# Performance work log

Measured on AMD Instinct MI355X. Metric: run time of the kernel, lower is better.

## Reference

```python
import jax, jax.numpy as jnp
import numpy as np

N = 100000
E = 3200000
D_IN = 128
HEADS = 4
OUT_CH = 64


def setup_inputs() -> dict:
    key = jax.random.key(0)
    kx, ke, kw, kb = jax.random.split(key, 4)
    x = jax.random.normal(kx, (N, D_IN), dtype=jnp.float32)
    edge_index = jax.random.randint(ke, (2, E), 0, N, dtype=jnp.int64)
    # nn.Linear(in_channels, out_channels*heads): weight [out, in] in torch; store as [in, out] for x @ W
    W = jax.random.normal(kw, (D_IN, OUT_CH * HEADS), dtype=jnp.float32) * (1.0 / np.sqrt(D_IN))
    b = jax.random.normal(kb, (OUT_CH * HEADS,), dtype=jnp.float32) * 0.01
    return {"x": x, "edge_index": edge_index, "W": W, "b": b}


def reference(x, edge_index, W, b):
    src, dst = edge_index[0], edge_index[1]
    n = x.shape[0]
    # scatter-add of gathered src features into dst rows (segment sum)
    agg = jax.ops.segment_sum(x[src], dst, num_segments=n)  # [N, D_IN]
    count = jax.ops.segment_sum(jnp.ones((src.shape[0], 1), x.dtype), dst, num_segments=n)  # [N, 1]
    agg = agg / (count + 1e-8)
    # linear on (x + agg); view to [N, heads*out_channels] is a no-op reshape
    return (x + agg) @ W + b
```

## Files before the change

### kernel.cpp

```cpp
#include <hip/hip_runtime.h>

#define N_NODES 100000
#define D_IN 128
#define D_OUT 256
#define NBLK 512
#define NBKT 2048
#define BSH  6
#define BNODES 64
#define NBUCKETS ((N_NODES + BNODES - 1) / BNODES)
#define CAP  3072

typedef __attribute__((ext_vector_type(8))) short short8_t;
typedef __attribute__((ext_vector_type(4))) float f32x4;

__device__ inline unsigned short f2bf_rne(float f) {
    unsigned u = __float_as_uint(f);
    u += 0x7fffu + ((u >> 16) & 1u);
    return (unsigned short)(u >> 16);
}

__global__ __launch_bounds__(256) void convert_kernel(
    const float* __restrict__ x, ushort* __restrict__ xb, int n4)
{
    int i = blockIdx.x * 256 + threadIdx.x;
    if (i < n4) {
        float4 v = ((const float4*)x)[i];
        ushort4 r;
        r.x = f2bf_rne(v.x); r.y = f2bf_rne(v.y);
        r.z = f2bf_rne(v.z); r.w = f2bf_rne(v.w);
        ((ushort4*)xb)[i] = r;
    }
}

__global__ __launch_bounds__(256) void wfrag_kernel(
    const float* __restrict__ W, short8_t* __restrict__ wfrag)
{
    int tid  = blockIdx.x * 256 + threadIdx.x;
    int lane = tid & 63;
    int fi   = tid >> 6;
    int ks   = fi >> 4, nt = fi & 15;
    int k0   = ks * 32 + (lane >> 4) * 8;
    int col  = nt * 16 + (lane & 15);
    short8_t v;
    #pragma unroll
    for (int e = 0; e < 8; e++)
        v[e] = (short)f2bf_rne(W[(size_t)(k0 + e) * D_OUT + col]);
    wfrag[tid] = v;
}

__global__ __launch_bounds__(256) void binA_hist(
    const int* __restrict__ dst, int* __restrict__ blockHist, int E, int chunk)
{
    __shared__ int h[NBKT];
    int b = blockIdx.x, t = threadIdx.x;
    for (int i = t; i < NBKT; i += 256) h[i] = 0;
    __syncthreads();
    int e0 = b * chunk, e1 = min(e0 + chunk, E);
    for (int e = e0 + t; e < e1; e += 256)
        atomicAdd(&h[dst[e] >> BSH], 1);
    __syncthreads();
    for (int i = t; i < NBKT; i += 256)
        blockHist[b * NBKT + i] = h[i];
}

__global__ __launch_bounds__(256) void binA_scan(
    int* __restrict__ blockHist, int* __restrict__ bucketTotal)
{
    __shared__ int wsum[4];
    int bucket = blockIdx.x;
    int t = threadIdx.x, lane = t & 63, w = t >> 6;
    int v0 = blockHist[(t * 2    ) * NBKT + bucket];
    int v1 = blockHist[(t * 2 + 1) * NBKT + bucket];
    int v = v0 + v1;
    int s = v;
    #pragma unroll
    for (int d = 1; d < 64; d <<= 1) {
        int u = __shfl_up(s, d);
        if (lane >= d) s += u;
    }
    if (lane == 63) wsum[w] = s;
    __syncthreads();
    int wo = 0;
    for (int j = 0; j < w; j++) wo += wsum[j];
    int excl = wo + s - v;
    blockHist[(t * 2    ) * NBKT + bucket] = excl;
    blockHist[(t * 2 + 1) * NBKT + bucket] = excl + v0;
    if (t == 255) {
        int tot = 0;
        for (int j = 0; j < 4; j++) tot += wsum[j];
        bucketTotal[bucket] = tot;
    }
}

__global__ __launch_bounds__(256) void binA_scanbase(
    const int* __restrict__ bucketTotal, int* __restrict__ bucketBase)
{
    __shared__ int wsum[4];
    int t = threadIdx.x, lane = t & 63, w = t >> 6;
    int i0 = t * 8;
    int a[8], v = 0;
    #pragma unroll
    for (int j = 0; j < 8; j++) { a[j] = bucketTotal[i0 + j]; v += a[j]; }
    int s = v;
    #pragma unroll
    for (int d = 1; d < 64; d <<= 1) {
        int u = __shfl_up(s, d);
        if (lane >= d) s += u;
    }
    if (lane == 63) wsum[w] = s;
    __syncthreads();
    int wo = 0;
    for (int j = 0; j < w; j++) wo += wsum[j];
    int excl = wo + s - v;
    #pragma unroll
    for (int j = 0; j < 8; j++) { bucketBase[i0 + j] = excl; excl += a[j]; }
}

__global__ __launch_bounds__(256) void binA_scatter(
    const int* __restrict__ src, const int* __restrict__ dst,
    const int* __restrict__ blockHist, const int* __restrict__ bucketBase,
    unsigned* __restrict__ pairs, int E, int chunk)
{
    __shared__ int offs[NBKT];
    int b = blockIdx.x, t = threadIdx.x;
    for (int i = t; i < NBKT; i += 256)
        offs[i] = bucketBase[i] + blockHist[b * NBKT + i];
    __syncthreads();
    int e0 = b * chunk, e1 = min(e0 + chunk, E);
    for (int e = e0 + t; e < e1; e += 256) {
        int d = dst[e];
        int bin = d >> BSH;
        int pos = atomicAdd(&offs[bin], 1);
        pairs[pos] = ((unsigned)(d & (BNODES - 1)) << 17) | (unsigned)src[e];
    }
}

__global__ __launch_bounds__(256) void binB_sort(
    unsigned* __restrict__ pairs, const int* __restrict__ bucketBase,
    int* __restrict__ offs_g, int* __restrict__ deg_g)
{
    __shared__ unsigned stage[CAP];
    __shared__ int hist[256];
    __shared__ int rank[256];
    __shared__ int wsum[4];

    int b = blockIdx.x, t = threadIdx.x, lane = t & 63, w = t >> 6;
    int e0 = bucketBase[b], e1 = bucketBase[b + 1];
    int cnt = e1 - e0;
    if (cnt > CAP) cnt = CAP;

    hist[t] = 0;
    __syncthreads();

    for (int i = t; i < cnt; i += 256) {
        unsigned p = pairs[e0 + i];
        stage[i] = p;
        atomicAdd(&hist[p >> 17], 1);
    }
    __syncthreads();

    int v = hist[t];
    int s = v;
    #pragma unroll
    for (int d = 1; d < 64; d <<= 1) {
        int u = __shfl_up(s, d);
        if (lane >= d) s += u;
    }
    if (lane == 63) wsum[w] = s;
    __syncthreads();
    int wo = 0;
    for (int j = 0; j < w; j++) wo += wsum[j];
    int excl = wo + s - v;

    int node = (b << BSH) + t;
    if (t < BNODES && node < N_NODES) {
        offs_g[node] = e0 + excl;
        deg_g[node]  = v;
    }
    rank[t] = excl;
    __syncthreads();

    for (int i = t; i < cnt; i += 256) {
        unsigned p = stage[i];
        int pos = atomicAdd(&rank[p >> 17], 1);
        pairs[e0 + pos] = p & 0x1FFFFu;
    }
}

template <bool USE_BF16>
__global__ __launch_bounds__(256) void fused_kernel(
    const float* __restrict__ x,
    const ushort* __restrict__ xb,
    const int* __restrict__ offs,
    const int* __restrict__ deg,
    const int* __restrict__ sorted_src,
    const short8_t* __restrict__ wfrag,
    const float* __restrict__ b,
    float* __restrict__ out)
{
    __shared__ __align__(16) ushort shb[16 * D_IN];

    int n0   = blockIdx.x * 16;
    int t    = threadIdx.x;
    int lane = t & 63;
    int w    = t >> 6;

    for (int nn = 0; nn < 4; nn++) {
        int nl = w * 4 + nn;
        int n  = n0 + nl;
        int start = offs[n];
        int d     = deg[n];
        float accx = 0.0f, accy = 0.0f;
        for (int base = 0; base < d; base += 64) {
            int m = d - base; if (m > 64) m = 64;
            int id = (lane < m) ? sorted_src[start + base + lane] : 0;
            int j = 0;
            for (; j + 4 <= m; j += 4) {
                int s0 = __builtin_amdgcn_readlane(id, j);
                int s1 = __builtin_amdgcn_readlane(id, j + 1);
                int s2 = __builtin_amdgcn_readlane(id, j + 2);
                int s3 = __builtin_amdgcn_readlane(id, j + 3);
                if (USE_BF16) {
                    ushort2 u0 = ((const ushort2*)(xb + (size_t)s0 * D_IN))[lane];
                    ushort2 u1 = ((const ushort2*)(xb + (size_t)s1 * D_IN))[lane];
                    ushort2 u2 = ((const ushort2*)(xb + (size_t)s2 * D_IN))[lane];
                    ushort2 u3 = ((const ushort2*)(xb + (size_t)s3 * D_IN))[lane];
                    accx += __uint_as_float((unsigned)u0.x << 16)
                          + __uint_as_float((unsigned)u1.x << 16)
                          + __uint_as_float((unsigned)u2.x << 16)
                          + __uint_as_float((unsigned)u3.x << 16);
                    accy += __uint_as_float((unsigned)u0.y << 16)
                          + __uint_as_float((unsigned)u1.y << 16)
                          + __uint_as_float((unsigned)u2.y << 16)
                          + __uint_as_float((unsigned)u3.y << 16);
                } else {
                    float2 v0 = ((const float2*)(x + (size_t)s0 * D_IN))[lane];
                    float2 v1 = ((const float2*)(x + (size_t)s1 * D_IN))[lane];
                    float2 v2 = ((const float2*)(x + (size_t)s2 * D_IN))[lane];
                    float2 v3 = ((const float2*)(x + (size_t)s3 * D_IN))[lane];
                    accx += v0.x + v1.x + v2.x + v3.x;
                    accy += v0.y + v1.y + v2.y + v3.y;
                }
            }
            for (; j < m; j++) {
                int s0 = __builtin_amdgcn_readlane(id, j);
                if (USE_BF16) {
                    ushort2 u0 = ((const ushort2*)(xb + (size_t)s0 * D_IN))[lane];
                    accx += __uint_as_float((unsigned)u0.x << 16);
                    accy += __uint_as_float((unsigned)u0.y << 16);
                } else {
                    float2 v0 = ((const float2*)(x + (size_t)s0 * D_IN))[lane];
                    accx += v0.x; accy += v0.y;
                }
            }
        }
        float invc = 1.0f / ((float)d + 1e-8f);
        float2 xv = ((const float2*)(x + (size_t)n * D_IN))[lane];
        float hx = xv.x + accx * invc;
        float hy = xv.y + accy * invc;
        unsigned hp = ((unsigned)f2bf_rne(hy) << 16) | (unsigned)f2bf_rne(hx);
        unsigned byteoff = ((unsigned)(nl * 256 + lane * 4)) ^ (((unsigned)nl & 7u) << 4);
        *(unsigned*)((char*)shb + byteoff) = hp;
    }
    __syncthreads();

    const int r  = lane & 15;
    const int hi = lane >> 4;

    short8_t afrag[4];
    #pragma unroll
    for (int ks = 0; ks < 4; ks++) {
        unsigned aoff = ((unsigned)(r * 256 + ks * 64 + hi * 16)) ^ (((unsigned)r & 7u) << 4);
        afrag[ks] = *(const short8_t*)((const char*)shb + aoff);
    }

    f32x4 zero = {0.0f, 0.0f, 0.0f, 0.0f};
    f32x4 acc0 = zero, acc1 = zero, acc2 = zero, acc3 = zero;
    const int nt0 = w * 4;
    #pragma unroll
    for (int ks = 0; ks < 4; ks++) {
        short8_t b0 = wfrag[(ks * 16 + nt0    ) * 64 + lane];
        short8_t b1 = wfrag[(ks * 16 + nt0 + 1) * 64 + lane];
        short8_t b2 = wfrag[(ks * 16 + nt0 + 2) * 64 + lane];
        short8_t b3 = wfrag[(ks * 16 + nt0 + 3) * 64 + lane];
        acc0 = __builtin_amdgcn_mfma_f32_16x16x32_bf16(afrag[ks], b0, acc0, 0, 0, 0);
        acc1 = __builtin_amdgcn_mfma_f32_16x16x32_bf16(afrag[ks], b1, acc1, 0, 0, 0);
        acc2 = __builtin_amdgcn_mfma_f32_16x16x32_bf16(afrag[ks], b2, acc2, 0, 0, 0);
        acc3 = __builtin_amdgcn_mfma_f32_16x16x32_bf16(afrag[ks], b3, acc3, 0, 0, 0);
    }

    #pragma unroll
    for (int nt = 0; nt < 4; nt++) {
        f32x4 a = (nt == 0) ? acc0 : (nt == 1) ? acc1 : (nt == 2) ? acc2 : acc3;
        int col = (nt0 + nt) * 16 + r;
        float bias = b[col];
        #pragma unroll
        for (int reg = 0; reg < 4; reg++) {
            int node = n0 + hi * 4 + reg;
            out[(size_t)node * D_OUT + col] = a[reg] + bias;
        }
    }
}

extern "C" void kernel_launch(void* const* d_in, const int* in_sizes, int n_in,
                              void* d_out, int out_size, void* d_ws, size_t ws_size,
                              hipStream_t stream)
{
    const float* x  = (const float*)d_in[0];
    const int*   ei = (const int*)d_in[1];
    const float* W  = (const float*)d_in[2];
    const float* b  = (const float*)d_in[3];
    float*       out = (float*)d_out;

    const int E = in_sizes[1] / 2;
    const int* src = ei;
    const int* dst = ei + E;
    const int chunk = (E + NBLK - 1) / NBLK;

    const size_t xb_bytes   = (size_t)N_NODES * D_IN * 2;
    const size_t pairs_b    = (size_t)E * 4;
    const size_t bh_b       = (size_t)NBLK * NBKT * 4;
    const size_t small_b    = (size_t)NBKT * 4;
    const size_t nodes_b    = (size_t)N_NODES * 4;
    const size_t wf_b       = (size_t)4096 * 16;
    const size_t need_bf16  = xb_bytes + pairs_b + bh_b + 2 * small_b
                            + 2 * nodes_b + wf_b;
    const bool use_bf16 = (ws_size >= need_bf16);

    char* p = (char*)d_ws;
    ushort* xb = nullptr;
    if (use_bf16) { xb = (ushort*)p; p += xb_bytes; }
    unsigned* pairs  = (unsigned*)p;  p += pairs_b;
    int* blockHist   = (int*)p;       p += bh_b;
    int* bucketTotal = (int*)p;       p += small_b;
    int* bucketBase  = (int*)p;       p += small_b;
    int* offs        = (int*)p;       p += nodes_b;
    int* deg         = (int*)p;       p += nodes_b;
    short8_t* wfrag  = (short8_t*)p;

    if (use_bf16) {
        int n4 = N_NODES * D_IN / 4;
        convert_kernel<<<dim3((n4 + 255) / 256), dim3(256), 0, stream>>>(x, xb, n4);
    }
    wfrag_kernel<<<dim3(16), dim3(256), 0, stream>>>(W, wfrag);

    binA_hist    <<<dim3(NBLK), dim3(256), 0, stream>>>(dst, blockHist, E, chunk);
    binA_scan    <<<dim3(NBKT), dim3(256), 0, stream>>>(blockHist, bucketTotal);
    binA_scanbase<<<dim3(1),    dim3(256), 0, stream>>>(bucketTotal, bucketBase);
    binA_scatter <<<dim3(NBLK), dim3(256), 0, stream>>>(
        src, dst, blockHist, bucketBase, pairs, E, chunk);
    binB_sort    <<<dim3(NBUCKETS), dim3(256), 0, stream>>>(
        pairs, bucketBase, offs, deg);

    if (use_bf16)
        fused_kernel<true><<<dim3(N_NODES / 16), dim3(256), 0, stream>>>(
            x, xb, offs, deg, (const int*)pairs, wfrag, b, out);
    else
        fused_kernel<false><<<dim3(N_NODES / 16), dim3(256), 0, stream>>>(
            x, xb, offs, deg, (const int*)pairs, wfrag, b, out);
}
```

Baseline: 408.7 us.

## Fuse per-bucket sort into aggregation kernel, one block per 64-node bucket

Removes the separate binB_sort kernel and does the per-bucket counting sort in LDS inside the fused aggregation+GEMM kernel. Each block now handles one 64-node bucket (16 nodes per wave) and no longer writes or rereads offs/deg arrays or the sorted pairs from global memory. In exchange, LDS use per block rises (CAP ints plus a 64x128 bf16 tile), which may lower occupancy, and the block count drops from 6250 to about 1563. Each wave now runs 16 MFMA column tiles with the B fragments loaded per tile.

```diff
diff --git a/kernel.cpp b/kernel.cpp
--- a/kernel.cpp
+++ b/kernel.cpp
@@ -135,85 +135,68 @@
     }
 }
 
-__global__ __launch_bounds__(256) void binB_sort(
-    unsigned* __restrict__ pairs, const int* __restrict__ bucketBase,
-    int* __restrict__ offs_g, int* __restrict__ deg_g)
-{
-    __shared__ unsigned stage[CAP];
-    __shared__ int hist[256];
-    __shared__ int rank[256];
-    __shared__ int wsum[4];
-
-    int b = blockIdx.x, t = threadIdx.x, lane = t & 63, w = t >> 6;
-    int e0 = bucketBase[b], e1 = bucketBase[b + 1];
-    int cnt = e1 - e0;
-    if (cnt > CAP) cnt = CAP;
-
-    hist[t] = 0;
-    __syncthreads();
-
-    for (int i = t; i < cnt; i += 256) {
-        unsigned p = pairs[e0 + i];
-        stage[i] = p;
-        atomicAdd(&hist[p >> 17], 1);
-    }
-    __syncthreads();
-
-    int v = hist[t];
-    int s = v;
-    #pragma unroll
-    for (int d = 1; d < 64; d <<= 1) {
-        int u = __shfl_up(s, d);
-        if (lane >= d) s += u;
-    }
-    if (lane == 63) wsum[w] = s;
-    __syncthreads();
-    int wo = 0;
-    for (int j = 0; j < w; j++) wo += wsum[j];
-    int excl = wo + s - v;
-
-    int node = (b << BSH) + t;
-    if (t < BNODES && node < N_NODES) {
-        offs_g[node] = e0 + excl;
-        deg_g[node]  = v;
-    }
-    rank[t] = excl;
-    __syncthreads();
-
-    for (int i = t; i < cnt; i += 256) {
-        unsigned p = stage[i];
-        int pos = atomicAdd(&rank[p >> 17], 1);
-        pairs[e0 + pos] = p & 0x1FFFFu;
-    }
-}
-
 template <bool USE_BF16>
 __global__ __launch_bounds__(256) void fused_kernel(
     const float* __restrict__ x,
     const ushort* __restrict__ xb,
-    const int* __restrict__ offs,
-    const int* __restrict__ deg,
-    const int* __restrict__ sorted_src,
+    const unsigned* __restrict__ pairs,
+    const int* __restrict__ bucketBase,
     const short8_t* __restrict__ wfrag,
     const float* __restrict__ b,
     float* __restrict__ out)
 {
-    __shared__ __align__(16) ushort shb[16 * D_IN];
-
-    int n0   = blockIdx.x * 16;
-    int t    = threadIdx.x;
-    int lane = t & 63;
-    int w    = t >> 6;
-
-    for (int nn = 0; nn < 4; nn++) {
-        int nl = w * 4 + nn;
+    __shared__ int srcSorted[CAP];
+    __shared__ __align__(16) ushort shb[BNODES * D_IN];
+    __shared__ int hist_l[BNODES];
+    __shared__ int offs_l[BNODES];
+    __shared__ int rank_l[BNODES];
+
+    const int t    = threadIdx.x;
+    const int lane = t & 63;
+    const int w    = t >> 6;
+    const int bkt  = blockIdx.x;
+    const int n0   = bkt << BSH;
+
+    const int e0 = bucketBase[bkt], e1 = bucketBase[bkt + 1];
+    int cnt = e1 - e0;
+    if (cnt > CAP) cnt = CAP;
+
+    if (t < BNODES) hist_l[t] = 0;
+    __syncthreads();
+
+    for (int i = t; i < cnt; i += 256)
+        atomicAdd(&hist_l[pairs[e0 + i] >> 17], 1);
+    __syncthreads();
+
+    if (t < 64) {
+        int v = hist_l[t];
+        int s = v;
+        #pragma unroll
+        for (int d = 1; d < 64; d <<= 1) {
+            int u = __shfl_up(s, d);
+            if (t >= d) s += u;
+        }
+        offs_l[t] = s - v;
+        rank_l[t] = s - v;
+    }
+    __syncthreads();
+
+    for (int i = t; i < cnt; i += 256) {
+        unsigned p = pairs[e0 + i];
+        int pos = atomicAdd(&rank_l[p >> 17], 1);
+        srcSorted[pos] = (int)(p & 0x1FFFFu);
+    }
+    __syncthreads();
+
+    for (int nn = 0; nn < 16; nn++) {
+        int nl = (w << 4) + nn;
         int n  = n0 + nl;
-        int start = offs[n];
-        int d     = deg[n];
+        int start = offs_l[nl];
+        int d     = hist_l[nl];
         float accx = 0.0f, accy = 0.0f;
         for (int base = 0; base < d; base += 64) {
             int m = d - base; if (m > 64) m = 64;
-            int id = (lane < m) ? sorted_src[start + base + lane] : 0;
+            int id = (lane < m) ? srcSorted[start + base + lane] : 0;
             int j = 0;
             for (; j + 4 <= m; j += 4) {
                 int s0 = __builtin_amdgcn_readlane(id, j);
@@ -254,10 +237,13 @@
                 }
             }
         }
-        float invc = 1.0f / ((float)d + 1e-8f);
-        float2 xv = ((const float2*)(x + (size_t)n * D_IN))[lane];
-        float hx = xv.x + accx * invc;
-        float hy = xv.y + accy * invc;
+        float hx = 0.0f, hy = 0.0f;
+        if (n < N_NODES) {
+            float invc = 1.0f / ((float)d + 1e-8f);
+            float2 xv = ((const float2*)(x + (size_t)n * D_IN))[lane];
+            hx = xv.x + accx * invc;
+            hy = xv.y + accy * invc;
+        }
         unsigned hp = ((unsigned)f2bf_rne(hy) << 16) | (unsigned)f2bf_rne(hx);
         unsigned byteoff = ((unsigned)(nl * 256 + lane * 4)) ^ (((unsigned)nl & 7u) << 4);
         *(unsigned*)((char*)shb + byteoff) = hp;
@@ -266,38 +252,30 @@
 
     const int r  = lane & 15;
     const int hi = lane >> 4;
+    const int rr = (w << 4) + r;
 
     short8_t afrag[4];
     #pragma unroll
     for (int ks = 0; ks < 4; ks++) {
-        unsigned aoff = ((unsigned)(r * 256 + ks * 64 + hi * 16)) ^ (((unsigned)r & 7u) << 4);
+        unsigned aoff = ((unsigned)(rr * 256 + ks * 64 + hi * 16)) ^ (((unsigned)rr & 7u) << 4);
         afrag[ks] = *(const short8_t*)((const char*)shb + aoff);
     }
 
-    f32x4 zero = {0.0f, 0.0f, 0.0f, 0.0f};
-    f32x4 acc0 = zero, acc1 = zero, acc2 = zero, acc3 = zero;
-    const int nt0 = w * 4;
-    #pragma unroll
-    for (int ks = 0; ks < 4; ks++) {
-        short8_t b0 = wfrag[(ks * 16 + nt0    ) * 64 + lane];
-        short8_t b1 = wfrag[(ks * 16 + nt0 + 1) * 64 + lane];
-        short8_t b2 = wfrag[(ks * 16 + nt0 + 2) * 64 + lane];
-        short8_t b3 = wfrag[(ks * 16 + nt0 + 3) * 64 + lane];
-        acc0 = __builtin_amdgcn_mfma_f32_16x16x32_bf16(afrag[ks], b0, acc0, 0, 0, 0);
-        acc1 = __builtin_amdgcn_mfma_f32_16x16x32_bf16(afrag[ks], b1, acc1, 0, 0, 0);
-        acc2 = __builtin_amdgcn_mfma_f32_16x16x32_bf16(afrag[ks], b2, acc2, 0, 0, 0);
-        acc3 = __builtin_amdgcn_mfma_f32_16x16x32_bf16(afrag[ks], b3, acc3, 0, 0, 0);
-    }
-
-    #pragma unroll
-    for (int nt = 0; nt < 4; nt++) {
-        f32x4 a = (nt == 0) ? acc0 : (nt == 1) ? acc1 : (nt == 2) ? acc2 : acc3;
-        int col = (nt0 + nt) * 16 + r;
+    #pragma unroll 4
+    for (int nt = 0; nt < 16; nt++) {
+        f32x4 acc = {0.0f, 0.0f, 0.0f, 0.0f};
+        #pragma unroll
+        for (int ks = 0; ks < 4; ks++) {
+            short8_t bf = wfrag[(ks * 16 + nt) * 64 + lane];
+            acc = __builtin_amdgcn_mfma_f32_16x16x32_bf16(afrag[ks], bf, acc, 0, 0, 0);
+        }
+        int col = nt * 16 + r;
         float bias = b[col];
         #pragma unroll
         for (int reg = 0; reg < 4; reg++) {
-            int node = n0 + hi * 4 + reg;
-            out[(size_t)node * D_OUT + col] = a[reg] + bias;
+            int node = n0 + (w << 4) + hi * 4 + reg;
+            if (node < N_NODES)
+                out[(size_t)node * D_OUT + col] = acc[reg] + bias;
         }
     }
 }
@@ -321,10 +299,8 @@
     const size_t pairs_b    = (size_t)E * 4;
     const size_t bh_b       = (size_t)NBLK * NBKT * 4;
     const size_t small_b    = (size_t)NBKT * 4;
-    const size_t nodes_b    = (size_t)N_NODES * 4;
     const size_t wf_b       = (size_t)4096 * 16;
-    const size_t need_bf16  = xb_bytes + pairs_b + bh_b + 2 * small_b
-                            + 2 * nodes_b + wf_b;
+    const size_t need_bf16  = xb_bytes + pairs_b + bh_b + 2 * small_b + wf_b;
     const bool use_bf16 = (ws_size >= need_bf16);
 
     char* p = (char*)d_ws;
@@ -334,8 +310,6 @@
     int* blockHist   = (int*)p;       p += bh_b;
     int* bucketTotal = (int*)p;       p += small_b;
     int* bucketBase  = (int*)p;       p += small_b;
-    int* offs        = (int*)p;       p += nodes_b;
-    int* deg         = (int*)p;       p += nodes_b;
     short8_t* wfrag  = (short8_t*)p;
 
     if (use_bf16) {
@@ -349,13 +323,11 @@
     binA_scanbase<<<dim3(1),    dim3(256), 0, stream>>>(bucketTotal, bucketBase);
     binA_scatter <<<dim3(NBLK), dim3(256), 0, stream>>>(
         src, dst, blockHist, bucketBase, pairs, E, chunk);
-    binB_sort    <<<dim3(NBUCKETS), dim3(256), 0, stream>>>(
-        pairs, bucketBase, offs, deg);
 
     if (use_bf16)
-        fused_kernel<true><<<dim3(N_NODES / 16), dim3(256), 0, stream>>>(
-            x, xb, offs, deg, (const int*)pairs, wfrag, b, out);
+        fused_kernel<true><<<dim3(NBUCKETS), dim3(256), 0, stream>>>(
+            x, xb, pairs, bucketBase, wfrag, b, out);
     else
-        fused_kernel<false><<<dim3(N_NODES / 16), dim3(256), 0, stream>>>(
-            x, xb, offs, deg, (const int*)pairs, wfrag, b, out);
-}
+        fused_kernel<false><<<dim3(NBUCKETS), dim3(256), 0, stream>>>(
+            x, xb, pairs, bucketBase, wfrag, b, out);
+}
```

Result: slower. 450.0 us (+10.1%).

## Replace two-level bucket sort with global-atomic counting sort for CSR build

Applied to the files above, without the earlier changes.

Replaces the two-pass bucket binning (per-block histograms, bucket scan, scatter, then in-LDS sort per bucket) with a direct CSR build. The new path counts degrees with global atomics, runs a three-stage prefix scan over nodes, and scatters src indices using per-node atomic cursors. This drops the large per-block histogram buffer and the LDS sort pass, but 3.2M global atomics on random addresses are added twice. The scatter writes are random and neighbour order within each node is nondeterministic, which can slightly change float summation order.

```diff
diff --git a/kernel.cpp b/kernel.cpp
--- a/kernel.cpp
+++ b/kernel.cpp
@@ -3,12 +3,8 @@
 #define N_NODES 100000
 #define D_IN 128
 #define D_OUT 256
-#define NBLK 512
-#define NBKT 2048
-#define BSH  6
-#define BNODES 64
-#define NBUCKETS ((N_NODES + BNODES - 1) / BNODES)
-#define CAP  3072
+#define NBLKN ((N_NODES + 255) / 256)
+#define EBLK 2048
 
 typedef __attribute__((ext_vector_type(8))) short short8_t;
 typedef __attribute__((ext_vector_type(4))) float f32x4;
@@ -48,30 +44,54 @@
     wfrag[tid] = v;
 }
 
-__global__ __launch_bounds__(256) void binA_hist(
-    const int* __restrict__ dst, int* __restrict__ blockHist, int E, int chunk)
-{
-    __shared__ int h[NBKT];
-    int b = blockIdx.x, t = threadIdx.x;
-    for (int i = t; i < NBKT; i += 256) h[i] = 0;
+__global__ __launch_bounds__(256) void zero_deg(int* __restrict__ deg)
+{
+    int i = blockIdx.x * 256 + threadIdx.x;
+    if (i < N_NODES) deg[i] = 0;
+}
+
+__global__ __launch_bounds__(256) void count_deg(
+    const int* __restrict__ dst, int* __restrict__ deg, int E)
+{
+    int stride = gridDim.x * 256;
+    for (int i = blockIdx.x * 256 + threadIdx.x; i < E; i += stride)
+        atomicAdd(&deg[dst[i]], 1);
+}
+
+__global__ __launch_bounds__(256) void scanA(
+    const int* __restrict__ deg, int* __restrict__ offs, int* __restrict__ bsum)
+{
+    __shared__ int wsum[4];
+    int b = blockIdx.x, t = threadIdx.x, lane = t & 63, w = t >> 6;
+    int n = b * 256 + t;
+    int v = (n < N_NODES) ? deg[n] : 0;
+    int s = v;
+    #pragma unroll
+    for (int d = 1; d < 64; d <<= 1) {
+        int u = __shfl_up(s, d);
+        if (lane >= d) s += u;
+    }
+    if (lane == 63) wsum[w] = s;
     __syncthreads();
-    int e0 = b * chunk, e1 = min(e0 + chunk, E);
-    for (int e = e0 + t; e < e1; e += 256)
-        atomicAdd(&h[dst[e] >> BSH], 1);
-    __syncthreads();
-    for (int i = t; i < NBKT; i += 256)
-        blockHist[b * NBKT + i] = h[i];
-}
-
-__global__ __launch_bounds__(256) void binA_scan(
-    int* __restrict__ blockHist, int* __restrict__ bucketTotal)
+    int wo = 0;
+    for (int j = 0; j < w; j++) wo += wsum[j];
+    if (n < N_NODES) offs[n] = wo + s - v;
+    if (t == 255) {
+        int tot = 0;
+        for (int j = 0; j < 4; j++) tot += wsum[j];
+        bsum[b] = tot;
+    }
+}
+
+__global__ __launch_bounds__(256) void scanB(
+    const int* __restrict__ bsum, int* __restrict__ bbase)
 {
     __shared__ int wsum[4];
-    int bucket = blockIdx.x;
     int t = threadIdx.x, lane = t & 63, w = t >> 6;
-    int v0 = blockHist[(t * 2    ) * NBKT + bucket];
-    int v1 = blockHist[(t * 2 + 1) * NBKT + bucket];
-    int v = v0 + v1;
+    int i0 = t * 2;
+    int a0 = (i0     < NBLKN) ? bsum[i0]     : 0;
+    int a1 = (i0 + 1 < NBLKN) ? bsum[i0 + 1] : 0;
+    int v = a0 + a1;
     int s = v;
     #pragma unroll
     for (int d = 1; d < 64; d <<= 1) {
@@ -83,107 +103,31 @@
     int wo = 0;
     for (int j = 0; j < w; j++) wo += wsum[j];
     int excl = wo + s - v;
-    blockHist[(t * 2    ) * NBKT + bucket] = excl;
-    blockHist[(t * 2 + 1) * NBKT + bucket] = excl + v0;
-    if (t == 255) {
-        int tot = 0;
-        for (int j = 0; j < 4; j++) tot += wsum[j];
-        bucketTotal[bucket] = tot;
-    }
-}
-
-__global__ __launch_bounds__(256) void binA_scanbase(
-    const int* __restrict__ bucketTotal, int* __restrict__ bucketBase)
-{
-    __shared__ int wsum[4];
-    int t = threadIdx.x, lane = t & 63, w = t >> 6;
-    int i0 = t * 8;
-    int a[8], v = 0;
-    #pragma unroll
-    for (int j = 0; j < 8; j++) { a[j] = bucketTotal[i0 + j]; v += a[j]; }
-    int s = v;
-    #pragma unroll
-    for (int d = 1; d < 64; d <<= 1) {
-        int u = __shfl_up(s, d);
-        if (lane >= d) s += u;
-    }
-    if (lane == 63) wsum[w] = s;
-    __syncthreads();
-    int wo = 0;
-    for (int j = 0; j < w; j++) wo += wsum[j];
-    int excl = wo + s - v;
-    #pragma unroll
-    for (int j = 0; j < 8; j++) { bucketBase[i0 + j] = excl; excl += a[j]; }
-}
-
-__global__ __launch_bounds__(256) void binA_scatter(
+    if (i0     < NBLKN) bbase[i0]     = excl;
+    if (i0 + 1 < NBLKN) bbase[i0 + 1] = excl + a0;
+}
+
+__global__ __launch_bounds__(256) void scanC(
+    int* __restrict__ offs, const int* __restrict__ bbase, int* __restrict__ cur)
+{
+    int b = blockIdx.x, t = threadIdx.x;
+    int n = b * 256 + t;
+    if (n < N_NODES) {
+        int o = offs[n] + bbase[b];
+        offs[n] = o;
+        cur[n]  = o;
+    }
+}
+
+__global__ __launch_bounds__(256) void scatter_csr(
     const int* __restrict__ src, const int* __restrict__ dst,
-    const int* __restrict__ blockHist, const int* __restrict__ bucketBase,
-    unsigned* __restrict__ pairs, int E, int chunk)
-{
-    __shared__ int offs[NBKT];
-    int b = blockIdx.x, t = threadIdx.x;
-    for (int i = t; i < NBKT; i += 256)
-        offs[i] = bucketBase[i] + blockHist[b * NBKT + i];
-    __syncthreads();
-    int e0 = b * chunk, e1 = min(e0 + chunk, E);
-    for (int e = e0 + t; e < e1; e += 256) {
-        int d = dst[e];
-        int bin = d >> BSH;
-        int pos = atomicAdd(&offs[bin], 1);
-        pairs[pos] = ((unsigned)(d & (BNODES - 1)) << 17) | (unsigned)src[e];
-    }
-}
-
-__global__ __launch_bounds__(256) void binB_sort(
-    unsigned* __restrict__ pairs, const int* __restrict__ bucketBase,
-    int* __restrict__ offs_g, int* __restrict__ deg_g)
-{
-    __shared__ unsigned stage[CAP];
-    __shared__ int hist[256];
-    __shared__ int rank[256];
-    __shared__ int wsum[4];
-
-    int b = blockIdx.x, t = threadIdx.x, lane = t & 63, w = t >> 6;
-    int e0 = bucketBase[b], e1 = bucketBase[b + 1];
-    int cnt = e1 - e0;
-    if (cnt > CAP) cnt = CAP;
-
-    hist[t] = 0;
-    __syncthreads();
-
-    for (int i = t; i < cnt; i += 256) {
-        unsigned p = pairs[e0 + i];
-        stage[i] = p;
-        atomicAdd(&hist[p >> 17], 1);
-    }
-    __syncthreads();
-
-    int v = hist[t];
-    int s = v;
-    #pragma unroll
-    for (int d = 1; d < 64; d <<= 1) {
-        int u = __shfl_up(s, d);
-        if (lane >= d) s += u;
-    }
-    if (lane == 63) wsum[w] = s;
-    __syncthreads();
-    int wo = 0;
-    for (int j = 0; j < w; j++) wo += wsum[j];
-    int excl = wo + s - v;
-
-    int node = (b << BSH) + t;
-    if (t < BNODES && node < N_NODES) {
-        offs_g[node] = e0 + excl;
-        deg_g[node]  = v;
-    }
-    rank[t] = excl;
-    __syncthreads();
-
-    for (int i = t; i < cnt; i += 256) {
-        unsigned p = stage[i];
-        int pos = atomicAdd(&rank[p >> 17], 1);
-        pairs[e0 + pos] = p & 0x1FFFFu;
+    int* __restrict__ cur, int* __restrict__ csr, int E)
+{
+    int stride = gridDim.x * 256;
+    for (int i = blockIdx.x * 256 + threadIdx.x; i < E; i += stride) {
+        int d = dst[i];
+        int pos = atomicAdd(&cur[d], 1);
+        csr[pos] = src[i];
     }
 }
 
@@ -315,28 +259,25 @@
     const int E = in_sizes[1] / 2;
     const int* src = ei;
     const int* dst = ei + E;
-    const int chunk = (E + NBLK - 1) / NBLK;
-
-    const size_t xb_bytes   = (size_t)N_NODES * D_IN * 2;
-    const size_t pairs_b    = (size_t)E * 4;
-    const size_t bh_b       = (size_t)NBLK * NBKT * 4;
-    const size_t small_b    = (size_t)NBKT * 4;
-    const size_t nodes_b    = (size_t)N_NODES * 4;
-    const size_t wf_b       = (size_t)4096 * 16;
-    const size_t need_bf16  = xb_bytes + pairs_b + bh_b + 2 * small_b
-                            + 2 * nodes_b + wf_b;
+
+    const size_t xb_bytes  = (size_t)N_NODES * D_IN * 2;
+    const size_t csr_b     = (size_t)E * 4;
+    const size_t nodes_b   = (size_t)N_NODES * 4;
+    const size_t bsum_b    = (size_t)512 * 4;
+    const size_t wf_b      = (size_t)4096 * 16;
+    const size_t need_bf16 = xb_bytes + csr_b + 3 * nodes_b + 2 * bsum_b + wf_b;
     const bool use_bf16 = (ws_size >= need_bf16);
 
     char* p = (char*)d_ws;
     ushort* xb = nullptr;
     if (use_bf16) { xb = (ushort*)p; p += xb_bytes; }
-    unsigned* pairs  = (unsigned*)p;  p += pairs_b;
-    int* blockHist   = (int*)p;       p += bh_b;
-    int* bucketTotal = (int*)p;       p += small_b;
-    int* bucketBase  = (int*)p;       p += small_b;
-    int* offs        = (int*)p;       p += nodes_b;
-    int* deg         = (int*)p;       p += nodes_b;
-    short8_t* wfrag  = (short8_t*)p;
+    int* csr   = (int*)p;  p += csr_b;
+    int* deg   = (int*)p;  p += nodes_b;
+    int* offs  = (int*)p;  p += nodes_b;
+    int* cur   = (int*)p;  p += nodes_b;
+    int* bsum  = (int*)p;  p += bsum_b;
+    int* bbase = (int*)p;  p += bsum_b;
+    short8_t* wfrag = (short8_t*)p;
 
     if (use_bf16) {
         int n4 = N_NODES * D_IN / 4;
@@ -344,18 +285,17 @@
     }
     wfrag_kernel<<<dim3(16), dim3(256), 0, stream>>>(W, wfrag);
 
-    binA_hist    <<<dim3(NBLK), dim3(256), 0, stream>>>(dst, blockHist, E, chunk);
-    binA_scan    <<<dim3(NBKT), dim3(256), 0, stream>>>(blockHist, bucketTotal);
-    binA_scanbase<<<dim3(1),    dim3(256), 0, stream>>>(bucketTotal, bucketBase);
-    binA_scatter <<<dim3(NBLK), dim3(256), 0, stream>>>(
-        src, dst, blockHist, bucketBase, pairs, E, chunk);
-    binB_sort    <<<dim3(NBUCKETS), dim3(256), 0, stream>>>(
-        pairs, bucketBase, offs, deg);
+    zero_deg   <<<dim3(NBLKN), dim3(256), 0, stream>>>(deg);
+    count_deg  <<<dim3(EBLK),  dim3(256), 0, stream>>>(dst, deg, E);
+    scanA      <<<dim3(NBLKN), dim3(256), 0, stream>>>(deg, offs, bsum);
+    scanB      <<<dim3(1),     dim3(256), 0, stream>>>(bsum, bbase);
+    scanC      <<<dim3(NBLKN), dim3(256), 0, stream>>>(offs, bbase, cur);
+    scatter_csr<<<dim3(EBLK),  dim3(256), 0, stream>>>(src, dst, cur, csr, E);
 
     if (use_bf16)
         fused_kernel<true><<<dim3(N_NODES / 16), dim3(256), 0, stream>>>(
-            x, xb, offs, deg, (const int*)pairs, wfrag, b, out);
+            x, xb, offs, deg, csr, wfrag, b, out);
     else
         fused_kernel<false><<<dim3(N_NODES / 16), dim3(256), 0, stream>>>(
-            x, xb, offs, deg, (const int*)pairs, wfrag, b, out);
-}
+            x, xb, offs, deg, csr, wfrag, b, out);
+}
```

Result: slower. 670.4 us (+64.0%).

## Use coarser 512-node buckets with fewer binning blocks for the edge sort

Applied to the files above, without the earlier changes.

The two-level counting sort of edges by destination now uses 256 buckets of 512 nodes each instead of 2048 buckets of 64 nodes, and 256 histogram blocks instead of 512. The histogram, scan and scatter kernels are simplified to one bucket per thread, and the per-bucket sort now handles 512 local nodes with a large LDS staging buffer. This cuts the block-histogram traffic and the scan work. In exchange the sort runs as only about 196 large blocks that use a lot of shared memory, and any bucket holding more than CAP edges gets truncated.

```diff
diff --git a/kernel.cpp b/kernel.cpp
--- a/kernel.cpp
+++ b/kernel.cpp
@@ -3,12 +3,12 @@
 #define N_NODES 100000
 #define D_IN 128
 #define D_OUT 256
-#define NBLK 512
-#define NBKT 2048
-#define BSH  6
-#define BNODES 64
+#define NBLK 256
+#define NBKT 256
+#define BSH  9
+#define BNODES 512
 #define NBUCKETS ((N_NODES + BNODES - 1) / BNODES)
-#define CAP  3072
+#define CAP  19456
 
 typedef __attribute__((ext_vector_type(8))) short short8_t;
 typedef __attribute__((ext_vector_type(4))) float f32x4;
@@ -53,14 +53,13 @@
 {
     __shared__ int h[NBKT];
     int b = blockIdx.x, t = threadIdx.x;
-    for (int i = t; i < NBKT; i += 256) h[i] = 0;
+    h[t] = 0;
     __syncthreads();
     int e0 = b * chunk, e1 = min(e0 + chunk, E);
     for (int e = e0 + t; e < e1; e += 256)
         atomicAdd(&h[dst[e] >> BSH], 1);
     __syncthreads();
-    for (int i = t; i < NBKT; i += 256)
-        blockHist[b * NBKT + i] = h[i];
+    blockHist[b * NBKT + t] = h[t];
 }
 
 __global__ __launch_bounds__(256) void binA_scan(
@@ -69,9 +68,7 @@
     __shared__ int wsum[4];
     int bucket = blockIdx.x;
     int t = threadIdx.x, lane = t & 63, w = t >> 6;
-    int v0 = blockHist[(t * 2    ) * NBKT + bucket];
-    int v1 = blockHist[(t * 2 + 1) * NBKT + bucket];
-    int v = v0 + v1;
+    int v = blockHist[t * NBKT + bucket];
     int s = v;
     #pragma unroll
     for (int d = 1; d < 64; d <<= 1) {
@@ -82,9 +79,7 @@
     __syncthreads();
     int wo = 0;
     for (int j = 0; j < w; j++) wo += wsum[j];
-    int excl = wo + s - v;
-    blockHist[(t * 2    ) * NBKT + bucket] = excl;
-    blockHist[(t * 2 + 1) * NBKT + bucket] = excl + v0;
+    blockHist[t * NBKT + bucket] = wo + s - v;
     if (t == 255) {
         int tot = 0;
         for (int j = 0; j < 4; j++) tot += wsum[j];
@@ -97,10 +92,7 @@
 {
     __shared__ int wsum[4];
     int t = threadIdx.x, lane = t & 63, w = t >> 6;
-    int i0 = t * 8;
-    int a[8], v = 0;
-    #pragma unroll
-    for (int j = 0; j < 8; j++) { a[j] = bucketTotal[i0 + j]; v += a[j]; }
+    int v = bucketTotal[t];
     int s = v;
     #pragma unroll
     for (int d = 1; d < 64; d <<= 1) {
@@ -111,9 +103,7 @@
     __syncthreads();
     int wo = 0;
     for (int j = 0; j < w; j++) wo += wsum[j];
-    int excl = wo + s - v;
-    #pragma unroll
-    for (int j = 0; j < 8; j++) { bucketBase[i0 + j] = excl; excl += a[j]; }
+    bucketBase[t] = wo + s - v;
 }
 
 __global__ __launch_bounds__(256) void binA_scatter(
@@ -123,8 +113,7 @@
 {
     __shared__ int offs[NBKT];
     int b = blockIdx.x, t = threadIdx.x;
-    for (int i = t; i < NBKT; i += 256)
-        offs[i] = bucketBase[i] + blockHist[b * NBKT + i];
+    offs[t] = bucketBase[t] + blockHist[b * NBKT + t];
     __syncthreads();
     int e0 = b * chunk, e1 = min(e0 + chunk, E);
     for (int e = e0 + t; e < e1; e += 256) {
@@ -140,8 +129,8 @@
     int* __restrict__ offs_g, int* __restrict__ deg_g)
 {
     __shared__ unsigned stage[CAP];
-    __shared__ int hist[256];
-    __shared__ int rank[256];
+    __shared__ int hist[BNODES];
+    __shared__ int rank[BNODES];
     __shared__ int wsum[4];
 
     int b = blockIdx.x, t = threadIdx.x, lane = t & 63, w = t >> 6;
@@ -149,7 +138,7 @@
     int cnt = e1 - e0;
     if (cnt > CAP) cnt = CAP;
 
-    hist[t] = 0;
+    hist[t] = 0; hist[t + 256] = 0;
     __syncthreads();
 
     for (int i = t; i < cnt; i += 256) {
@@ -159,7 +148,8 @@
     }
     __syncthreads();
 
-    int v = hist[t];
+    int a0 = hist[t * 2], a1 = hist[t * 2 + 1];
+    int v = a0 + a1;
     int s = v;
     #pragma unroll
     for (int d = 1; d < 64; d <<= 1) {
@@ -172,12 +162,17 @@
     for (int j = 0; j < w; j++) wo += wsum[j];
     int excl = wo + s - v;
 
-    int node = (b << BSH) + t;
-    if (t < BNODES && node < N_NODES) {
+    rank[t * 2]     = excl;
+    rank[t * 2 + 1] = excl + a0;
+    int node = (b << BSH) + t * 2;
+    if (node < N_NODES) {
         offs_g[node] = e0 + excl;
-        deg_g[node]  = v;
-    }
-    rank[t] = excl;
+        deg_g[node]  = a0;
+    }
+    if (node + 1 < N_NODES) {
+        offs_g[node + 1] = e0 + excl + a0;
+        deg_g[node + 1]  = a1;
+    }
     __syncthreads();
 
     for (int i = t; i < cnt; i += 256) {
```

Result: no change. 405.8 us (-0.7%).
